# Optimization experiments

Hardware: AMD Instinct MI355X
Metric: run time of the kernel (lower is better)

## Reference

```python
import jax, jax.numpy as jnp
import numpy as np
import math

B, N, H, TDIM, K, R = 32, 4096, 256, 128, 2, 2


def setup_inputs() -> dict:
    key = jax.random.key(0)
    ks = jax.random.split(key, 12)
    s = 1.0 / math.sqrt(H)
    gain = 1.414
    return {
        "x": jax.random.normal(ks[0], (B, N), jnp.float32),
        "t": jax.random.uniform(ks[1], (B,), jnp.float32),
        # scaled so repeated L@x stays O(1) over Chebyshev hops
        "laplacian": jax.random.normal(ks[2], (N, N), jnp.float32) / math.sqrt(N),
        "w_g1": jax.random.normal(ks[3], (1, H, K + 1), jnp.float32) * gain / math.sqrt(1 + H),
        "w_g2": jax.random.normal(ks[4], (H, 1, K + 1), jnp.float32) * gain / math.sqrt(1 + H),
        "w_t1": jax.random.normal(ks[5], (TDIM, H), jnp.float32) / math.sqrt(TDIM),
        "b_t1": jnp.zeros((H,), jnp.float32),
        "w_t2": jax.random.normal(ks[6], (H, H), jnp.float32) * s,
        "b_t2": jnp.zeros((H,), jnp.float32),
        "w_map": jax.random.normal(ks[7], (N, H), jnp.float32) / math.sqrt(N),
        "b_map": jnp.zeros((H,), jnp.float32),
        "res_w": jax.random.normal(ks[8], (R, 3, H, H), jnp.float32) * s,
        "res_b": jnp.zeros((R, 3, H), jnp.float32),
        "w_o1": jax.random.normal(ks[9], (H, H), jnp.float32) * s,
        "b_o1": jnp.zeros((H,), jnp.float32),
        "w_o2": jax.random.normal(ks[10], (H, N), jnp.float32) * s,
        "b_o2": jnp.zeros((N,), jnp.float32),
    }


def timestep_embedding(t, dim, max_period=10000):
    half = dim // 2  # dim is even here
    freqs = jnp.exp(-math.log(max_period) * jnp.arange(half, dtype=t.dtype) / half)
    args = t[:, None] * freqs[None, :]  # [B, half]
    return jnp.concatenate([jnp.cos(args), jnp.sin(args)], axis=-1)  # [B, dim]


def gcn_layer(L, x, w, conv_order):
    xs = [x]
    h = x
    for _ in range(conv_order):
        h = jnp.einsum('mn,bnc->bmc', L, h)  # sparse-style Laplacian propagation (dense here)
        xs.append(h)
    X = jnp.stack(xs, axis=-1)  # [B, N, C, K+1]
    return jnp.einsum('bnik,iok->bno', X, w)


def reference(x, t, laplacian, w_g1, w_g2, w_t1, b_t1, w_t2, b_t2,
              w_map, b_map, res_w, res_b, w_o1, b_o1, w_o2, b_o2):
    silu = jax.nn.silu
    # time embedding path: sinusoidal -> Linear -> SiLU -> Linear
    temb = timestep_embedding(t, TDIM)
    t_out = silu(temb @ w_t1 + b_t1) @ w_t2 + b_t2  # [B, H]
    # GCNBlock: two Chebyshev GCN layers (GCNLayer.forward applies no activation)
    g = gcn_layer(laplacian, x[:, :, None], w_g1, K)  # [B, N, H]
    g = gcn_layer(laplacian, g, w_g2, K)[..., 0]      # [B, N]
    # ResNet_FC on the node signal
    h = g @ w_map + b_map  # [B, H]
    inv_sqrt2 = 1.0 / math.sqrt(2.0)
    for r in range(R):
        z = h
        for i in range(3):
            z = silu(z @ res_w[r, i] + res_b[r, i])
        h = (h + z) * inv_sqrt2
    # output head with time conditioning
    out = silu((h + t_out) @ w_o1 + b_o1) @ w_o2 + b_o2  # [B, N]
    return out
```

## Files before the change

### kernel.cpp

```cpp
#include <hip/hip_runtime.h>
#include <hip/hip_bf16.h>

typedef __bf16 bf16x8 __attribute__((ext_vector_type(8)));
typedef __bf16 bf16x4 __attribute__((ext_vector_type(4)));
typedef float  f32x4  __attribute__((ext_vector_type(4)));


static constexpr size_t WS_A     = 0;
static constexpr size_t WS_TOUT  = 1024;
static constexpr size_t WS_Z1    = 65536;
static constexpr size_t WS_ZSTR  = 524288;
static constexpr size_t WS_H0    = WS_Z1 + 4 * WS_ZSTR;
static constexpr size_t WS_G2F   = WS_H0 + 32768;
static constexpr size_t WS_UB    = WS_G2F + 524288;
static constexpr size_t WS_WMAPT = 2752512;
static constexpr size_t WS_WO2T  = WS_WMAPT + 2097152;

__device__ __forceinline__ f32x4 mfma16(bf16x8 a, bf16x8 b, f32x4 c) {
    return __builtin_amdgcn_mfma_f32_16x16x32_bf16(a, b, c, 0, 0, 0);
}

__device__ __forceinline__ bf16x8 cvt8(const float* p) {
    f32x4 lo = *(const f32x4*)p;
    f32x4 hi = *(const f32x4*)(p + 4);
    bf16x8 r;
    r[0] = (__bf16)lo[0]; r[1] = (__bf16)lo[1]; r[2] = (__bf16)lo[2]; r[3] = (__bf16)lo[3];
    r[4] = (__bf16)hi[0]; r[5] = (__bf16)hi[1]; r[6] = (__bf16)hi[2]; r[7] = (__bf16)hi[3];
    return r;
}

__device__ __forceinline__ float silu_f(float x) { return x / (1.0f + __expf(-x)); }

__device__ __forceinline__ void transpose_tile(const float* __restrict__ src, int sstride,
                                               __bf16* __restrict__ dst, int dstride,
                                               int r0, int c0, float* sh, int tid) {
    const int r = tid >> 3, cg = (tid & 7) * 4;
    f32x4 v = *(const f32x4*)(src + (size_t)(r0 + r) * sstride + c0 + cg);
    sh[r * 33 + cg + 0] = v[0];
    sh[r * 33 + cg + 1] = v[1];
    sh[r * 33 + cg + 2] = v[2];
    sh[r * 33 + cg + 3] = v[3];
    __syncthreads();
    bf16x4 o;
    o[0] = (__bf16)sh[(cg + 0) * 33 + r];
    o[1] = (__bf16)sh[(cg + 1) * 33 + r];
    o[2] = (__bf16)sh[(cg + 2) * 33 + r];
    o[3] = (__bf16)sh[(cg + 3) * 33 + r];
    *(bf16x4*)(dst + (size_t)(c0 + r) * dstride + r0 + cg) = o;
}

__global__ __launch_bounds__(256) void prep_kernel(
    const float* __restrict__ t,
    const float* __restrict__ w_g1, const float* __restrict__ w_g2,
    const float* __restrict__ w_t1, const float* __restrict__ b_t1,
    const float* __restrict__ w_t2, const float* __restrict__ b_t2,
    const float* __restrict__ w_map, const float* __restrict__ w_o2,
    char* __restrict__ ws)
{
    __shared__ float sh[1056];
    const int bi = blockIdx.x, tid = threadIdx.x;
    if (bi == 0) {
        if (tid < 9) {
            const int k1 = tid / 3, k2 = tid % 3;
            float s = 0.f;
            for (int h = 0; h < 256; ++h) s += w_g1[h * 3 + k1] * w_g2[h * 3 + k2];
            sh[tid] = s;
        }
        __syncthreads();
        if (tid == 0) {
            float* a = (float*)(ws + WS_A);
            a[0] = sh[0];
            a[1] = sh[1] + sh[3];
            a[2] = sh[2] + sh[4] + sh[6];
            a[3] = sh[5] + sh[7];
            a[4] = sh[8];
        }
    } else if (bi < 33) {
        const int b = bi - 1;
        float* t_out = (float*)(ws + WS_TOUT);
        if (tid < 64) {
            float fr = __expf(-9.210340371976184f * (float)tid * (1.0f / 64.0f));
            float ang = t[b] * fr;
            sh[tid]      = __cosf(ang);
            sh[64 + tid] = __sinf(ang);
        }
        __syncthreads();
        float acc = b_t1[tid];
        for (int j = 0; j < 128; ++j) acc += sh[j] * w_t1[j * 256 + tid];
        sh[128 + tid] = silu_f(acc);
        __syncthreads();
        float acc2 = b_t2[tid];
        for (int j = 0; j < 256; ++j) acc2 += sh[128 + j] * w_t2[j * 256 + tid];
        t_out[b * 256 + tid] = acc2;
    } else if (bi < 553) {
        f32x4* p = (f32x4*)(ws + WS_Z1 + (size_t)(bi - 33) * 4096);
        f32x4 z = {0.f, 0.f, 0.f, 0.f};
        p[tid] = z;
    } else if (bi < 1577) {
        const int ti = bi - 553;
        transpose_tile(w_map, 256, (__bf16*)(ws + WS_WMAPT), 4096,
                       (ti >> 3) * 32, (ti & 7) * 32, sh, tid);
    } else {
        const int ti = bi - 1577;
        transpose_tile(w_o2, 4096, (__bf16*)(ws + WS_WO2T), 256,
                       (ti & 7) * 32, (ti >> 3) * 32, sh, tid);
    }
}

__global__ __launch_bounds__(512) void hop_kernel(
    const float* __restrict__ L, const float* __restrict__ zin,
    float* __restrict__ zout)
{
    __shared__ float red[8][32][33];
    const int bi = blockIdx.x, tid = threadIdx.x;
    const int wave = tid >> 6, lane = tid & 63;
    const int l15 = lane & 15, q = lane >> 4;
    const int m0 = (bi >> 2) * 32;
    const int kbase = (bi & 3) * 1024 + wave * 128;

    const float* a0p = L + (size_t)(m0 + l15) * 4096;
    const float* a1p = a0p + (size_t)16 * 4096;
    const float* b0p = zin + (size_t)l15 * 4096;
    const float* b1p = zin + (size_t)(l15 + 16) * 4096;

    f32x4 acc00 = {0,0,0,0}, acc01 = {0,0,0,0}, acc10 = {0,0,0,0}, acc11 = {0,0,0,0};
#pragma unroll
    for (int ks = 0; ks < 4; ++ks) {
        const int k = kbase + ks * 32 + q * 8;
        bf16x8 a0 = cvt8(a0p + k);
        bf16x8 a1 = cvt8(a1p + k);
        bf16x8 b0 = cvt8(b0p + k);
        bf16x8 b1 = cvt8(b1p + k);
        acc00 = mfma16(a0, b0, acc00);
        acc01 = mfma16(a0, b1, acc01);
        acc10 = mfma16(a1, b0, acc10);
        acc11 = mfma16(a1, b1, acc11);
    }
#pragma unroll
    for (int r = 0; r < 4; ++r) {
        red[wave][q * 4 + r][l15]           = acc00[r];
        red[wave][q * 4 + r][l15 + 16]      = acc01[r];
        red[wave][16 + q * 4 + r][l15]      = acc10[r];
        red[wave][16 + q * 4 + r][l15 + 16] = acc11[r];
    }
    __syncthreads();
#pragma unroll
    for (int o = tid; o < 1024; o += 512) {
        const int m = o & 31, bcol = o >> 5;
        float v = 0.f;
#pragma unroll
        for (int w = 0; w < 8; ++w) v += red[w][m][bcol];
        atomicAdd(zout + (size_t)bcol * 4096 + m0 + m, v);
    }
}

__global__ __launch_bounds__(256) void combine_kernel(
    const float* __restrict__ x,
    const float* __restrict__ z1, const float* __restrict__ z2,
    const float* __restrict__ z3, const float* __restrict__ z4,
    const float* __restrict__ a, float* __restrict__ g2)
{
    const int i = blockIdx.x * 256 + threadIdx.x;
    const float a0 = a[0], a1 = a[1], a2 = a[2], a3 = a[3], a4 = a[4];
    f32x4 r = a0 * ((const f32x4*)x)[i] + a1 * ((const f32x4*)z1)[i]
            + a2 * ((const f32x4*)z2)[i] + a3 * ((const f32x4*)z3)[i]
            + a4 * ((const f32x4*)z4)[i];
    ((f32x4*)g2)[i] = r;
}

__global__ __launch_bounds__(256) void map_gemm_kernel(
    const float* __restrict__ g2, const __bf16* __restrict__ w_mapT,
    float* __restrict__ h0)
{
    __shared__ float red[4][16][32];
    const int bi = blockIdx.x, tid = threadIdx.x;
    const int wave = tid >> 6, lane = tid & 63;
    const int l15 = lane & 15, q = lane >> 4;
    const int btile = bi & 1;
    const int hp = (bi >> 1) & 7;
    const int kc = bi >> 4;
    const int kbase = kc * 512 + wave * 128;

    const float*  ap  = g2 + (size_t)(btile * 16 + l15) * 4096;
    const __bf16* bp0 = w_mapT + (size_t)(hp * 32 + l15) * 4096;
    const __bf16* bp1 = w_mapT + (size_t)(hp * 32 + 16 + l15) * 4096;

    f32x4 acc0 = {0,0,0,0}, acc1 = {0,0,0,0};
#pragma unroll
    for (int ks = 0; ks < 4; ++ks) {
        const int k = kbase + ks * 32 + q * 8;
        bf16x8 a  = cvt8(ap + k);
        bf16x8 b0 = *(const bf16x8*)(bp0 + k);
        bf16x8 b1 = *(const bf16x8*)(bp1 + k);
        acc0 = mfma16(a, b0, acc0);
        acc1 = mfma16(a, b1, acc1);
    }
#pragma unroll
    for (int r = 0; r < 4; ++r) {
        red[wave][q * 4 + r][l15]      = acc0[r];
        red[wave][q * 4 + r][l15 + 16] = acc1[r];
    }
    __syncthreads();
    const int b_l = tid >> 4, hl = tid & 15;
#pragma unroll
    for (int s = 0; s < 2; ++s) {
        const int h_l = hl + s * 16;
        float v = red[0][b_l][h_l] + red[1][b_l][h_l] + red[2][b_l][h_l] + red[3][b_l][h_l];
        atomicAdd(h0 + (size_t)(btile * 16 + b_l) * 256 + hp * 32 + h_l, v);
    }
}

__global__ __launch_bounds__(1024) void resnet_kernel(
    const float* __restrict__ h0, const float* __restrict__ b_map,
    const float* __restrict__ res_w, const float* __restrict__ res_b,
    const float* __restrict__ t_out, const float* __restrict__ w_o1,
    const float* __restrict__ b_o1, __bf16* __restrict__ u_b)
{
    __shared__ float zs[256];
    __shared__ float part[4][256];
    const int b = blockIdx.x, tid = threadIdx.x;
    const int col = tid & 255, kg = tid >> 8;

    float hv = 0.f;
    if (kg == 0) {
        hv = h0[b * 256 + col] + b_map[col];
        zs[col] = hv;
    }
    __syncthreads();

#pragma unroll
    for (int r = 0; r < 2; ++r) {
        for (int i = 0; i < 3; ++i) {
            const float* W = res_w + ((size_t)(r * 3 + i) << 16) + (size_t)kg * 64 * 256 + col;
            const float* zp = zs + kg * 64;
            float a0 = 0, a1 = 0, a2 = 0, a3 = 0;
#pragma unroll
            for (int j = 0; j < 64; j += 4) {
                a0 += zp[j]     * W[(j)     * 256];
                a1 += zp[j + 1] * W[(j + 1) * 256];
                a2 += zp[j + 2] * W[(j + 2) * 256];
                a3 += zp[j + 3] * W[(j + 3) * 256];
            }
            part[kg][col] = (a0 + a1) + (a2 + a3);
            __syncthreads();
            if (kg == 0) {
                zs[col] = silu_f(res_b[(r * 3 + i) * 256 + col]
                                 + part[0][col] + part[1][col] + part[2][col] + part[3][col]);
            }
            __syncthreads();
        }
        if (kg == 0) {
            hv = (hv + zs[col]) * 0.70710678118654752f;
            zs[col] = hv;
        }
        __syncthreads();
    }

    if (kg == 0) zs[col] = hv + t_out[b * 256 + col];
    __syncthreads();
    {
        const float* W = w_o1 + (size_t)kg * 64 * 256 + col;
        const float* zp = zs + kg * 64;
        float a0 = 0, a1 = 0, a2 = 0, a3 = 0;
#pragma unroll
        for (int j = 0; j < 64; j += 4) {
            a0 += zp[j]     * W[(j)     * 256];
            a1 += zp[j + 1] * W[(j + 1) * 256];
            a2 += zp[j + 2] * W[(j + 2) * 256];
            a3 += zp[j + 3] * W[(j + 3) * 256];
        }
        part[kg][col] = (a0 + a1) + (a2 + a3);
    }
    __syncthreads();
    if (kg == 0) {
        u_b[b * 256 + col] = (__bf16)silu_f(b_o1[col]
            + part[0][col] + part[1][col] + part[2][col] + part[3][col]);
    }
}

__global__ __launch_bounds__(256) void out_gemm_kernel(
    const __bf16* __restrict__ u_b, const __bf16* __restrict__ w_o2T,
    const float* __restrict__ b_o2, float* __restrict__ out)
{
    const int tid = threadIdx.x;
    const int wave = tid >> 6, lane = tid & 63;
    const int l15 = lane & 15, q = lane >> 4;
    const int g = blockIdx.x * 4 + wave;
    const int btile = g & 1;
    const int n0 = (g >> 1) * 32;

    const __bf16* ap  = u_b + (size_t)(btile * 16 + l15) * 256;
    const __bf16* bp0 = w_o2T + (size_t)(n0 + l15) * 256;
    const __bf16* bp1 = w_o2T + (size_t)(n0 + 16 + l15) * 256;

    f32x4 acc0 = {0,0,0,0}, acc1 = {0,0,0,0};
#pragma unroll
    for (int ks = 0; ks < 8; ++ks) {
        const int k = ks * 32 + q * 8;
        bf16x8 a  = *(const bf16x8*)(ap + k);
        bf16x8 b0 = *(const bf16x8*)(bp0 + k);
        bf16x8 b1 = *(const bf16x8*)(bp1 + k);
        acc0 = mfma16(a, b0, acc0);
        acc1 = mfma16(a, b1, acc1);
    }
    const int row = btile * 16 + q * 4;
    const int na = n0 + l15, nb = n0 + 16 + l15;
#pragma unroll
    for (int r = 0; r < 4; ++r) {
        out[(size_t)(row + r) * 4096 + na] = acc0[r] + b_o2[na];
        out[(size_t)(row + r) * 4096 + nb] = acc1[r] + b_o2[nb];
    }
}

extern "C" void kernel_launch(void* const* d_in, const int* in_sizes, int n_in,
                              void* d_out, int out_size, void* d_ws, size_t ws_size,
                              hipStream_t stream)
{
    (void)in_sizes; (void)n_in; (void)out_size; (void)ws_size;
    const float* x     = (const float*)d_in[0];
    const float* t     = (const float*)d_in[1];
    const float* L     = (const float*)d_in[2];
    const float* w_g1  = (const float*)d_in[3];
    const float* w_g2  = (const float*)d_in[4];
    const float* w_t1  = (const float*)d_in[5];
    const float* b_t1  = (const float*)d_in[6];
    const float* w_t2  = (const float*)d_in[7];
    const float* b_t2  = (const float*)d_in[8];
    const float* w_map = (const float*)d_in[9];
    const float* b_map = (const float*)d_in[10];
    const float* res_w = (const float*)d_in[11];
    const float* res_b = (const float*)d_in[12];
    const float* w_o1  = (const float*)d_in[13];
    const float* b_o1  = (const float*)d_in[14];
    const float* w_o2  = (const float*)d_in[15];
    const float* b_o2  = (const float*)d_in[16];
    float* out = (float*)d_out;
    char* ws = (char*)d_ws;

    float* a_c  = (float*)(ws + WS_A);
    float* tout = (float*)(ws + WS_TOUT);
    float* z1   = (float*)(ws + WS_Z1);
    float* z2   = (float*)(ws + WS_Z1 + WS_ZSTR);
    float* z3   = (float*)(ws + WS_Z1 + 2 * WS_ZSTR);
    float* z4   = (float*)(ws + WS_Z1 + 3 * WS_ZSTR);
    float* h0   = (float*)(ws + WS_H0);
    float* g2   = (float*)(ws + WS_G2F);
    __bf16* u_b    = (__bf16*)(ws + WS_UB);
    __bf16* w_mapT = (__bf16*)(ws + WS_WMAPT);
    __bf16* w_o2T  = (__bf16*)(ws + WS_WO2T);

    prep_kernel<<<2601, 256, 0, stream>>>(t, w_g1, w_g2, w_t1, b_t1, w_t2, b_t2,
                                          w_map, w_o2, ws);
    hop_kernel<<<512, 512, 0, stream>>>(L, x,  z1);
    hop_kernel<<<512, 512, 0, stream>>>(L, z1, z2);
    hop_kernel<<<512, 512, 0, stream>>>(L, z2, z3);
    hop_kernel<<<512, 512, 0, stream>>>(L, z3, z4);
    combine_kernel<<<128, 256, 0, stream>>>(x, z1, z2, z3, z4, a_c, g2);
    map_gemm_kernel<<<128, 256, 0, stream>>>(g2, w_mapT, h0);
    resnet_kernel<<<32, 1024, 0, stream>>>(h0, b_map, res_w, res_b, tout, w_o1, b_o1, u_b);
    out_gemm_kernel<<<64, 256, 0, stream>>>(u_b, w_o2T, b_o2, out);
}
```

Before: 238.6 us.

## Cache bf16 Laplacian on first hop and reuse it for later Chebyshev hops

The first hop converts the fp32 Laplacian to bf16, writes it to workspace, and later hops read that bf16 copy, roughly halving Laplacian traffic for three of four hops. Hop kernels now give each block a full K range of 16 rows, so outputs are written directly instead of through atomics, and the zero-fill of z buffers is dropped. Activations (x, z, g2) are also kept in bf16 so no conversion happens inside the GEMM loops. The cost is an extra 32MB write in hop1, and each block now processes more K per wave with fewer blocks.

```diff
diff --git a/kernel.cpp b/kernel.cpp
--- a/kernel.cpp
+++ b/kernel.cpp
@@ -8,13 +8,17 @@
 
 static constexpr size_t WS_A     = 0;
 static constexpr size_t WS_TOUT  = 1024;
-static constexpr size_t WS_Z1    = 65536;
+static constexpr size_t WS_H0    = 65536;
+static constexpr size_t WS_UB    = 131072;
+static constexpr size_t WS_XB    = 262144;
+static constexpr size_t WS_G2B   = 524288;
+static constexpr size_t WS_ZB1   = 1048576;
+static constexpr size_t WS_ZBSTR = 262144;
+static constexpr size_t WS_Z1    = 2097152;
 static constexpr size_t WS_ZSTR  = 524288;
-static constexpr size_t WS_H0    = WS_Z1 + 4 * WS_ZSTR;
-static constexpr size_t WS_G2F   = WS_H0 + 32768;
-static constexpr size_t WS_UB    = WS_G2F + 524288;
-static constexpr size_t WS_WMAPT = 2752512;
-static constexpr size_t WS_WO2T  = WS_WMAPT + 2097152;
+static constexpr size_t WS_WMAPT = 4194304;
+static constexpr size_t WS_WO2T  = 6291456;
+static constexpr size_t WS_LB    = 8388608;
 
 __device__ __forceinline__ f32x4 mfma16(bf16x8 a, bf16x8 b, f32x4 c) {
     return __builtin_amdgcn_mfma_f32_16x16x32_bf16(a, b, c, 0, 0, 0);
@@ -50,7 +54,7 @@
 }
 
 __global__ __launch_bounds__(256) void prep_kernel(
-    const float* __restrict__ t,
+    const float* __restrict__ x, const float* __restrict__ t,
     const float* __restrict__ w_g1, const float* __restrict__ w_g2,
     const float* __restrict__ w_t1, const float* __restrict__ b_t1,
     const float* __restrict__ w_t2, const float* __restrict__ b_t2,
@@ -60,20 +64,30 @@
     __shared__ float sh[1056];
     const int bi = blockIdx.x, tid = threadIdx.x;
     if (bi == 0) {
-        if (tid < 9) {
-            const int k1 = tid / 3, k2 = tid % 3;
-            float s = 0.f;
-            for (int h = 0; h < 256; ++h) s += w_g1[h * 3 + k1] * w_g2[h * 3 + k2];
-            sh[tid] = s;
+        const float g10 = w_g1[tid * 3 + 0], g11 = w_g1[tid * 3 + 1], g12 = w_g1[tid * 3 + 2];
+        const float g20 = w_g2[tid * 3 + 0], g21 = w_g2[tid * 3 + 1], g22 = w_g2[tid * 3 + 2];
+        float p[9] = {g10 * g20, g10 * g21, g10 * g22,
+                      g11 * g20, g11 * g21, g11 * g22,
+                      g12 * g20, g12 * g21, g12 * g22};
+        const int wv = tid >> 6, ln = tid & 63;
+#pragma unroll
+        for (int j = 0; j < 9; ++j) {
+            float v = p[j];
+#pragma unroll
+            for (int off = 32; off > 0; off >>= 1) v += __shfl_down(v, off);
+            if (ln == 0) sh[wv * 9 + j] = v;
         }
         __syncthreads();
         if (tid == 0) {
+            float s[9];
+#pragma unroll
+            for (int j = 0; j < 9; ++j) s[j] = sh[j] + sh[9 + j] + sh[18 + j] + sh[27 + j];
             float* a = (float*)(ws + WS_A);
-            a[0] = sh[0];
-            a[1] = sh[1] + sh[3];
-            a[2] = sh[2] + sh[4] + sh[6];
-            a[3] = sh[5] + sh[7];
-            a[4] = sh[8];
+            a[0] = s[0];
+            a[1] = s[1] + s[3];
+            a[2] = s[2] + s[4] + s[6];
+            a[3] = s[5] + s[7];
+            a[4] = s[8];
         }
     } else if (bi < 33) {
         const int b = bi - 1;
@@ -92,65 +106,106 @@
         float acc2 = b_t2[tid];
         for (int j = 0; j < 256; ++j) acc2 += sh[128 + j] * w_t2[j * 256 + tid];
         t_out[b * 256 + tid] = acc2;
-    } else if (bi < 553) {
-        f32x4* p = (f32x4*)(ws + WS_Z1 + (size_t)(bi - 33) * 4096);
+    } else if (bi < 41) {
+        f32x4* p = (f32x4*)(ws + WS_H0);
         f32x4 z = {0.f, 0.f, 0.f, 0.f};
-        p[tid] = z;
-    } else if (bi < 1577) {
-        const int ti = bi - 553;
+        p[(bi - 33) * 256 + tid] = z;
+    } else if (bi < 105) {
+        const int e = ((bi - 41) * 256 + tid) * 8;
+        *(bf16x8*)((__bf16*)(ws + WS_XB) + e) = cvt8(x + e);
+    } else if (bi < 1129) {
+        const int ti = bi - 105;
         transpose_tile(w_map, 256, (__bf16*)(ws + WS_WMAPT), 4096,
                        (ti >> 3) * 32, (ti & 7) * 32, sh, tid);
     } else {
-        const int ti = bi - 1577;
+        const int ti = bi - 1129;
         transpose_tile(w_o2, 4096, (__bf16*)(ws + WS_WO2T), 256,
                        (ti & 7) * 32, (ti >> 3) * 32, sh, tid);
     }
 }
 
-__global__ __launch_bounds__(512) void hop_kernel(
-    const float* __restrict__ L, const float* __restrict__ zin,
-    float* __restrict__ zout)
-{
-    __shared__ float red[8][32][33];
+__global__ __launch_bounds__(1024) void hop1_kernel(
+    const float* __restrict__ L, const __bf16* __restrict__ xb,
+    float* __restrict__ zout, __bf16* __restrict__ zb_out,
+    __bf16* __restrict__ Lb)
+{
+    __shared__ float red[16][16][33];
     const int bi = blockIdx.x, tid = threadIdx.x;
     const int wave = tid >> 6, lane = tid & 63;
     const int l15 = lane & 15, q = lane >> 4;
-    const int m0 = (bi >> 2) * 32;
-    const int kbase = (bi & 3) * 1024 + wave * 128;
-
-    const float* a0p = L + (size_t)(m0 + l15) * 4096;
-    const float* a1p = a0p + (size_t)16 * 4096;
-    const float* b0p = zin + (size_t)l15 * 4096;
-    const float* b1p = zin + (size_t)(l15 + 16) * 4096;
-
-    f32x4 acc00 = {0,0,0,0}, acc01 = {0,0,0,0}, acc10 = {0,0,0,0}, acc11 = {0,0,0,0};
-#pragma unroll
-    for (int ks = 0; ks < 4; ++ks) {
+    const int m0 = bi * 16;
+    const int kbase = wave * 256;
+
+    const float*  lp  = L  + (size_t)(m0 + l15) * 4096;
+    __bf16*       lbp = Lb + (size_t)(m0 + l15) * 4096;
+    const __bf16* b0p = xb + (size_t)l15 * 4096;
+    const __bf16* b1p = xb + (size_t)(l15 + 16) * 4096;
+
+    f32x4 acc0 = {0,0,0,0}, acc1 = {0,0,0,0};
+#pragma unroll
+    for (int ks = 0; ks < 8; ++ks) {
         const int k = kbase + ks * 32 + q * 8;
-        bf16x8 a0 = cvt8(a0p + k);
-        bf16x8 a1 = cvt8(a1p + k);
-        bf16x8 b0 = cvt8(b0p + k);
-        bf16x8 b1 = cvt8(b1p + k);
-        acc00 = mfma16(a0, b0, acc00);
-        acc01 = mfma16(a0, b1, acc01);
-        acc10 = mfma16(a1, b0, acc10);
-        acc11 = mfma16(a1, b1, acc11);
+        bf16x8 a  = cvt8(lp + k);
+        *(bf16x8*)(lbp + k) = a;
+        bf16x8 b0 = *(const bf16x8*)(b0p + k);
+        bf16x8 b1 = *(const bf16x8*)(b1p + k);
+        acc0 = mfma16(a, b0, acc0);
+        acc1 = mfma16(a, b1, acc1);
     }
 #pragma unroll
     for (int r = 0; r < 4; ++r) {
-        red[wave][q * 4 + r][l15]           = acc00[r];
-        red[wave][q * 4 + r][l15 + 16]      = acc01[r];
-        red[wave][16 + q * 4 + r][l15]      = acc10[r];
-        red[wave][16 + q * 4 + r][l15 + 16] = acc11[r];
-    }
-    __syncthreads();
-#pragma unroll
-    for (int o = tid; o < 1024; o += 512) {
-        const int m = o & 31, bcol = o >> 5;
+        red[wave][q * 4 + r][l15]      = acc0[r];
+        red[wave][q * 4 + r][l15 + 16] = acc1[r];
+    }
+    __syncthreads();
+    if (tid < 512) {
+        const int m = tid & 15, b = tid >> 4;
         float v = 0.f;
 #pragma unroll
-        for (int w = 0; w < 8; ++w) v += red[w][m][bcol];
-        atomicAdd(zout + (size_t)bcol * 4096 + m0 + m, v);
+        for (int w = 0; w < 16; ++w) v += red[w][m][b];
+        zout[(size_t)b * 4096 + m0 + m] = v;
+        zb_out[(size_t)b * 4096 + m0 + m] = (__bf16)v;
+    }
+}
+
+__global__ __launch_bounds__(1024) void hop_bf_kernel(
+    const __bf16* __restrict__ Lb, const __bf16* __restrict__ zb_in,
+    float* __restrict__ zout, __bf16* __restrict__ zb_out)
+{
+    __shared__ float red[16][16][33];
+    const int bi = blockIdx.x, tid = threadIdx.x;
+    const int wave = tid >> 6, lane = tid & 63;
+    const int l15 = lane & 15, q = lane >> 4;
+    const int m0 = bi * 16;
+    const int kbase = wave * 256;
+
+    const __bf16* ap  = Lb + (size_t)(m0 + l15) * 4096;
+    const __bf16* b0p = zb_in + (size_t)l15 * 4096;
+    const __bf16* b1p = zb_in + (size_t)(l15 + 16) * 4096;
+
+    f32x4 acc0 = {0,0,0,0}, acc1 = {0,0,0,0};
+#pragma unroll
+    for (int ks = 0; ks < 8; ++ks) {
+        const int k = kbase + ks * 32 + q * 8;
+        bf16x8 a  = *(const bf16x8*)(ap + k);
+        bf16x8 b0 = *(const bf16x8*)(b0p + k);
+        bf16x8 b1 = *(const bf16x8*)(b1p + k);
+        acc0 = mfma16(a, b0, acc0);
+        acc1 = mfma16(a, b1, acc1);
+    }
+#pragma unroll
+    for (int r = 0; r < 4; ++r) {
+        red[wave][q * 4 + r][l15]      = acc0[r];
+        red[wave][q * 4 + r][l15 + 16] = acc1[r];
+    }
+    __syncthreads();
+    if (tid < 512) {
+        const int m = tid & 15, b = tid >> 4;
+        float v = 0.f;
+#pragma unroll
+        for (int w = 0; w < 16; ++w) v += red[w][m][b];
+        zout[(size_t)b * 4096 + m0 + m] = v;
+        if (zb_out) zb_out[(size_t)b * 4096 + m0 + m] = (__bf16)v;
     }
 }
 
@@ -158,18 +213,20 @@
     const float* __restrict__ x,
     const float* __restrict__ z1, const float* __restrict__ z2,
     const float* __restrict__ z3, const float* __restrict__ z4,
-    const float* __restrict__ a, float* __restrict__ g2)
+    const float* __restrict__ a, __bf16* __restrict__ g2b)
 {
     const int i = blockIdx.x * 256 + threadIdx.x;
     const float a0 = a[0], a1 = a[1], a2 = a[2], a3 = a[3], a4 = a[4];
     f32x4 r = a0 * ((const f32x4*)x)[i] + a1 * ((const f32x4*)z1)[i]
             + a2 * ((const f32x4*)z2)[i] + a3 * ((const f32x4*)z3)[i]
             + a4 * ((const f32x4*)z4)[i];
-    ((f32x4*)g2)[i] = r;
+    bf16x4 o;
+    o[0] = (__bf16)r[0]; o[1] = (__bf16)r[1]; o[2] = (__bf16)r[2]; o[3] = (__bf16)r[3];
+    ((bf16x4*)g2b)[i] = o;
 }
 
 __global__ __launch_bounds__(256) void map_gemm_kernel(
-    const float* __restrict__ g2, const __bf16* __restrict__ w_mapT,
+    const __bf16* __restrict__ g2b, const __bf16* __restrict__ w_mapT,
     float* __restrict__ h0)
 {
     __shared__ float red[4][16][32];
@@ -181,7 +238,7 @@
     const int kc = bi >> 4;
     const int kbase = kc * 512 + wave * 128;
 
-    const float*  ap  = g2 + (size_t)(btile * 16 + l15) * 4096;
+    const __bf16* ap  = g2b + (size_t)(btile * 16 + l15) * 4096;
     const __bf16* bp0 = w_mapT + (size_t)(hp * 32 + l15) * 4096;
     const __bf16* bp1 = w_mapT + (size_t)(hp * 32 + 16 + l15) * 4096;
 
@@ -189,7 +246,7 @@
 #pragma unroll
     for (int ks = 0; ks < 4; ++ks) {
         const int k = kbase + ks * 32 + q * 8;
-        bf16x8 a  = cvt8(ap + k);
+        bf16x8 a  = *(const bf16x8*)(ap + k);
         bf16x8 b0 = *(const bf16x8*)(bp0 + k);
         bf16x8 b1 = *(const bf16x8*)(bp1 + k);
         acc0 = mfma16(a, b0, acc0);
@@ -337,26 +394,31 @@
     float* out = (float*)d_out;
     char* ws = (char*)d_ws;
 
-    float* a_c  = (float*)(ws + WS_A);
-    float* tout = (float*)(ws + WS_TOUT);
-    float* z1   = (float*)(ws + WS_Z1);
-    float* z2   = (float*)(ws + WS_Z1 + WS_ZSTR);
-    float* z3   = (float*)(ws + WS_Z1 + 2 * WS_ZSTR);
-    float* z4   = (float*)(ws + WS_Z1 + 3 * WS_ZSTR);
-    float* h0   = (float*)(ws + WS_H0);
-    float* g2   = (float*)(ws + WS_G2F);
-    __bf16* u_b    = (__bf16*)(ws + WS_UB);
+    float*  a_c  = (float*)(ws + WS_A);
+    float*  tout = (float*)(ws + WS_TOUT);
+    float*  h0   = (float*)(ws + WS_H0);
+    __bf16* u_b  = (__bf16*)(ws + WS_UB);
+    __bf16* xb   = (__bf16*)(ws + WS_XB);
+    __bf16* g2b  = (__bf16*)(ws + WS_G2B);
+    __bf16* zb1  = (__bf16*)(ws + WS_ZB1);
+    __bf16* zb2  = (__bf16*)(ws + WS_ZB1 + WS_ZBSTR);
+    __bf16* zb3  = (__bf16*)(ws + WS_ZB1 + 2 * WS_ZBSTR);
+    float*  z1   = (float*)(ws + WS_Z1);
+    float*  z2   = (float*)(ws + WS_Z1 + WS_ZSTR);
+    float*  z3   = (float*)(ws + WS_Z1 + 2 * WS_ZSTR);
+    float*  z4   = (float*)(ws + WS_Z1 + 3 * WS_ZSTR);
     __bf16* w_mapT = (__bf16*)(ws + WS_WMAPT);
     __bf16* w_o2T  = (__bf16*)(ws + WS_WO2T);
-
-    prep_kernel<<<2601, 256, 0, stream>>>(t, w_g1, w_g2, w_t1, b_t1, w_t2, b_t2,
+    __bf16* Lb     = (__bf16*)(ws + WS_LB);
+
+    prep_kernel<<<2153, 256, 0, stream>>>(x, t, w_g1, w_g2, w_t1, b_t1, w_t2, b_t2,
                                           w_map, w_o2, ws);
-    hop_kernel<<<512, 512, 0, stream>>>(L, x,  z1);
-    hop_kernel<<<512, 512, 0, stream>>>(L, z1, z2);
-    hop_kernel<<<512, 512, 0, stream>>>(L, z2, z3);
-    hop_kernel<<<512, 512, 0, stream>>>(L, z3, z4);
-    combine_kernel<<<128, 256, 0, stream>>>(x, z1, z2, z3, z4, a_c, g2);
-    map_gemm_kernel<<<128, 256, 0, stream>>>(g2, w_mapT, h0);
+    hop1_kernel<<<256, 1024, 0, stream>>>(L, xb, z1, zb1, Lb);
+    hop_bf_kernel<<<256, 1024, 0, stream>>>(Lb, zb1, z2, zb2);
+    hop_bf_kernel<<<256, 1024, 0, stream>>>(Lb, zb2, z3, zb3);
+    hop_bf_kernel<<<256, 1024, 0, stream>>>(Lb, zb3, z4, nullptr);
+    combine_kernel<<<128, 256, 0, stream>>>(x, z1, z2, z3, z4, a_c, g2b);
+    map_gemm_kernel<<<128, 256, 0, stream>>>(g2b, w_mapT, h0);
     resnet_kernel<<<32, 1024, 0, stream>>>(h0, b_map, res_w, res_b, tout, w_o1, b_o1, u_b);
     out_gemm_kernel<<<64, 256, 0, stream>>>(u_b, w_o2T, b_o2, out);
 }
```

Result: faster. 229.2 us (-4.0%).
